# Kernel tuning notes

Measured on AMD Instinct MI355X. Metric: run time of the kernel, lower is better.

## Reference

```python
import jax, jax.numpy as jnp
import numpy as np

KH, KW = 2, 2          # kernel_size
STH, STW = 2, 2        # stride
NW = KH * KW           # num wires (qubits) per patch
DIM = 2 ** NW          # Hilbert-space dim = 16


def setup_inputs() -> dict:
    key = jax.random.key(0)
    k1, k2 = jax.random.split(key)
    x = jax.random.normal(k1, (32, 4, 64, 64), dtype=jnp.float32)
    # learned parameter: [in_channels, out_channels//numwires, 2^NW, 2^NW]
    params = jax.random.normal(k2, (4, 8, DIM, DIM), dtype=jnp.float32)
    return {"x": x, "params": params}


def _extract_patches(x):
    # x: [B, C, H, W] -> [B, C, px, py, KH*KW] (row-major kh,kw ordering,
    # matching patches.permute(0,1,4,5,2,3).flatten(4) in the original)
    B, C, H, W = x.shape
    px = (H - KH) // STH + 1
    py = (W - KW) // STW + 1
    rows = (jnp.arange(px) * STH)[:, None] + jnp.arange(KH)  # [px, KH]
    cols = (jnp.arange(py) * STW)[:, None] + jnp.arange(KW)  # [py, KW]
    p = x[:, :, rows][:, :, :, :, cols]        # [B, C, px, KH, py, KW]
    p = p.transpose(0, 1, 2, 4, 3, 5)          # [B, C, px, py, KH, KW]
    return p.reshape(B, C, px, py, NW), px, py


def _forward(x, params):
    B, C, H, W = x.shape
    p, px, py = _extract_patches(x)
    M = B * px * py
    theta = p.transpose(1, 0, 2, 3, 4).reshape(C, M, NW)  # 'b c px py i -> c (b px py) i'

    # Encode: the original builds the full tensor-product of per-wire RX
    # matrices and contracts with |0...0>, which selects row 0 of the Kronecker
    # product. Row 0 of RX(theta) is [cos(t/2), -i sin(t/2)], so the encoded
    # state is the Kronecker product of the per-wire row-0 vectors (same math,
    # without materializing the [C,M,16,16] unitary).
    half = theta * 0.5
    v = (jnp.cos(half).astype(jnp.complex64)[..., None] * jnp.array([1.0, 0.0], jnp.complex64)
         + jnp.sin(half).astype(jnp.complex64)[..., None] * jnp.array([0.0, -1.0j], jnp.complex64))  # [C,M,NW,2]
    state = v[:, :, 0]                                     # [C, M, 2]
    for w in range(1, NW):
        state = (state[..., :, None] * v[:, :, w][..., None, :]).reshape(C, M, -1)
    # state: [C, M, DIM]

    # Skew-Hermitian generator: real part antisymmetric, imag part symmetric.
    sym = params + params.swapaxes(-1, -2)
    asym = params - params.swapaxes(-1, -2)
    SH = asym.astype(jnp.complex64) + 1j * sym.astype(jnp.complex64)  # [C, D, DIM, DIM]
    U = jax.vmap(jax.vmap(jax.scipy.linalg.expm))(SH)                 # [C, D, DIM, DIM]

    y = jnp.einsum('cdij,cmi->cdmj', U, state)  # [C, D, M, DIM]

    # Decode: per-wire marginal probabilities -> <sigma_z>-style expectation -> acos
    probs = (y * jnp.conj(y)).real              # [C, D, M, DIM]
    D = probs.shape[1]
    outs = []
    for j in range(NW):
        marg = probs.reshape(C, D, M, 2 ** j, 2, 2 ** (NW - j - 1)).sum(axis=(3, 5))  # [C,D,M,2]
        outs.append(jnp.arccos(marg[..., 0] - marg[..., 1]))
    out = jnp.stack(outs, -1)                   # [C, D, M, NW]
    out = out.sum(0)                            # [D, M, NW]  (sum over in_channels)

    # 'c (b px py) (x y) -> b (c x y) px py' with c=D, x=KH, y=KW
    out = out.reshape(D, B, px, py, KH, KW).transpose(1, 0, 4, 5, 2, 3)
    return out.reshape(B, D * KH * KW, px, py)  # [B, out_channels, px, py]


def reference(x, params):
    return _forward(x, params)
```

## Files before the change

### kernel.cpp

```cpp
#include <hip/hip_runtime.h>
#include <math.h>


#define TAYLOR_N 9

typedef __attribute__((ext_vector_type(8)))  short bf16x8;
typedef __attribute__((ext_vector_type(16))) float f32x16;

__device__ __forceinline__ unsigned bfr(float x) {
    unsigned u = __float_as_uint(x);
    return (u + 0x7FFFu + ((u >> 16) & 1u)) >> 16;
}

__global__ __launch_bounds__(256) void prep_kernel(const float* __restrict__ params,
                                                   unsigned* __restrict__ wfrag) {
    __shared__ float2 X[256];
    __shared__ float2 P0[256];
    __shared__ float2 P1[256];
    __shared__ float red[256];
    __shared__ float srow[16];
    __shared__ int ssexp;

    const int bid = blockIdx.x;
    const int tid = threadIdx.x;
    const int i = tid >> 4, j = tid & 15;

    const float* pm = params + bid * 256;
    float pij = pm[i * 16 + j];
    float pji = pm[j * 16 + i];
    float ar = pij - pji;
    float ai = pij + pji;
    red[tid] = fabsf(ar) + fabsf(ai);
    __syncthreads();
    if (j == 0) {
        float s = 0.f;
        for (int t = 0; t < 16; ++t) s += red[i * 16 + t];
        srow[i] = s;
    }
    __syncthreads();
    if (tid == 0) {
        float mx = 0.f;
        for (int t = 0; t < 16; ++t) mx = fmaxf(mx, srow[t]);
        int se = 0;
        while (mx > 0.5f && se < 40) { mx *= 0.5f; se++; }
        ssexp = se;
    }
    __syncthreads();
    const int sexp = ssexp;
    const float scale = exp2f((float)(-sexp));
    const float xr = ar * scale, xi = ai * scale;
    X[tid] = make_float2(xr, xi);
    float2 p = make_float2(xr / TAYLOR_N + ((i == j) ? 1.f : 0.f), xi / TAYLOR_N);
    P0[tid] = p;
    __syncthreads();

    float2 Xr[16];
    #pragma unroll
    for (int t = 0; t < 16; ++t) Xr[t] = X[i * 16 + t];

    float2* cur = P0;
    float2* nxt = P1;
    for (int k = TAYLOR_N - 1; k >= 1; --k) {
        float accr = 0.f, acci = 0.f;
        #pragma unroll
        for (int t = 0; t < 16; ++t) {
            float2 a = Xr[t];
            float2 bb = cur[t * 16 + j];
            accr += a.x * bb.x - a.y * bb.y;
            acci += a.x * bb.y + a.y * bb.x;
        }
        float inv = 1.f / (float)k;
        float2 np = make_float2(accr * inv + ((i == j) ? 1.f : 0.f), acci * inv);
        __syncthreads();
        nxt[tid] = np;
        __syncthreads();
        float2* tmp = cur; cur = nxt; nxt = tmp;
    }
    for (int sq = 0; sq < sexp; ++sq) {
        float accr = 0.f, acci = 0.f;
        #pragma unroll
        for (int t = 0; t < 16; ++t) {
            float2 a = cur[i * 16 + t];
            float2 bb = cur[t * 16 + j];
            accr += a.x * bb.x - a.y * bb.y;
            acci += a.x * bb.y + a.y * bb.x;
        }
        __syncthreads();
        nxt[tid] = make_float2(accr, acci);
        __syncthreads();
        float2* tmp = cur; cur = nxt; nxt = tmp;
    }
    float2 e = cur[tid];
    int pc = __popc(i) & 3;
    float2 o;
    if (pc == 0)      o = make_float2( e.x,  e.y);
    else if (pc == 1) o = make_float2( e.y, -e.x);
    else if (pc == 2) o = make_float2(-e.x, -e.y);
    else              o = make_float2(-e.y,  e.x);
    __syncthreads();
    X[(tid & 15) * 16 + (tid >> 4)] = o;
    __syncthreads();

    {
        const int lane = tid & 63;
        const int pr = tid >> 6;
        const int row = lane & 31;
        const int kh = lane >> 5;
        const int k0 = kh * 8 + pr * 2;
        float v0, v1;
        if (row < 16) { v0 = X[row * 16 + k0].x; v1 = X[row * 16 + k0 + 1].x; }
        else          { v0 = X[(row - 16) * 16 + k0].y; v1 = X[(row - 16) * 16 + k0 + 1].y; }
        unsigned base = (unsigned)(bid * 64 + lane) * 4u;
        wfrag[base + pr] = bfr(v0) | (bfr(v1) << 16);
    }
}

__device__ __forceinline__ float acos_fast(float t) {
    float ax = fabsf(t);
    float p = fmaf(ax, -0.0187293f, 0.0742610f);
    p = fmaf(ax, p, -0.2121144f);
    p = fmaf(ax, p, 1.5707288f);
    float f = sqrtf(1.0f - ax) * p;
    return (t >= 0.f) ? f : (3.14159265358979f - f);
}

__global__ __launch_bounds__(256)
__attribute__((amdgpu_waves_per_eu(2, 4)))
void qconv_kernel(const float* __restrict__ x,
                  const unsigned* __restrict__ wfrag,
                  float* __restrict__ out) {
    const int tid = threadIdx.x;
    const int lane = tid & 63;
    const int s = lane & 31;
    const int hi = lane >> 5;
    const int wave = blockIdx.x * 4 + (tid >> 6);
    const int msite = wave >> 1;
    const int dh = wave & 1;
    const int m = msite * 32 + s;
    const int b = m >> 10, ix = (m >> 5) & 31, iy = m & 31;

    const bf16x8* wf = (const bf16x8*)wfrag;

    bf16x8 bhi[4], blo[4];
    #pragma unroll
    for (int c = 0; c < 4; ++c) {
        const float* xc = x + (((b * 4 + c) * 64 + 2 * ix) * 64 + 2 * iy);
        float2 xa = *(const float2*)xc;
        float2 xb = *(const float2*)(xc + 64);
        float sn0, cs0, sn1, cs1, sn2, cs2, sn3, cs3;
        __sincosf(xa.x * 0.5f, &sn0, &cs0);
        __sincosf(xa.y * 0.5f, &sn1, &cs1);
        __sincosf(xb.x * 0.5f, &sn2, &cs2);
        __sincosf(xb.y * 0.5f, &sn3, &cs3);
        float f0 = hi ? sn0 : cs0;
        float g0 = f0 * cs1, g1 = f0 * sn1;
        float h0 = g0 * cs2, h1 = g0 * sn2, h2 = g1 * cs2, h3 = g1 * sn2;
        float r[8];
        r[0] = h0 * cs3; r[1] = h0 * sn3; r[2] = h1 * cs3; r[3] = h1 * sn3;
        r[4] = h2 * cs3; r[5] = h2 * sn3; r[6] = h3 * cs3; r[7] = h3 * sn3;
        #pragma unroll
        for (int e = 0; e < 8; ++e) {
            unsigned hb = bfr(r[e]);
            bhi[c][e] = (short)hb;
            blo[c][e] = (short)bfr(r[e] - __uint_as_float(hb << 16));
        }
    }

    const float sgn1 = hi ? -1.f : 1.f;
    const f32x16 z = {0.f,0.f,0.f,0.f,0.f,0.f,0.f,0.f,
                      0.f,0.f,0.f,0.f,0.f,0.f,0.f,0.f};

    #pragma unroll 1
    for (int dd = 0; dd < 4; ++dd) {
        const int d = dh * 4 + dd;
        float accA = 0.f, accB = 0.f;
        #pragma unroll
        for (int c = 0; c < 4; ++c) {
            const int cd = c * 8 + d;
            bf16x8 ahi = wf[cd * 64 + lane];
            f32x16 acc = __builtin_amdgcn_mfma_f32_32x32x16_bf16(ahi, blo[c], z, 0, 0, 0);
            acc = __builtin_amdgcn_mfma_f32_32x32x16_bf16(ahi, bhi[c], acc, 0, 0, 0);
            float q[8];
            #pragma unroll
            for (int i = 0; i < 8; ++i)
                q[i] = fmaf(acc[i], acc[i], acc[8 + i] * acc[8 + i]);
            float e01 = q[0] + q[1], o01 = q[0] - q[1];
            float e23 = q[2] + q[3], o23 = q[2] - q[3];
            float e45 = q[4] + q[5], o45 = q[4] - q[5];
            float e67 = q[6] + q[7], o67 = q[6] - q[7];
            float A  = e01 + e23, B2a = e01 - e23, A3a = o01 + o23;
            float C  = e45 + e67, B2b = e45 - e67, A3b = o45 + o67;
            float S   = A + C;
            float pw0 = A - C;
            float pw1 = sgn1 * S;
            float pw2 = B2a + B2b;
            float pw3 = A3a + A3b;
            float sendA = hi ? pw0 : pw2, myA = hi ? pw2 : pw0;
            float sendB = hi ? pw1 : pw3, myB = hi ? pw3 : pw1;
            float tA = myA + __shfl_xor(sendA, 32);
            float tB = myB + __shfl_xor(sendB, 32);
            tA = fminf(fmaxf(tA, -1.f), 1.f);
            tB = fminf(fmaxf(tB, -1.f), 1.f);
            accA += acos_fast(tA);
            accB += acos_fast(tB);
        }
        float* ob = out + ((b * 32 + d * 4 + 2 * hi) * 32 + ix) * 32 + iy;
        ob[0]    = accA;
        ob[1024] = accB;
    }
}

extern "C" void kernel_launch(void* const* d_in, const int* in_sizes, int n_in,
                              void* d_out, int out_size, void* d_ws, size_t ws_size,
                              hipStream_t stream) {
    const float* x = (const float*)d_in[0];
    const float* params = (const float*)d_in[1];
    float* out = (float*)d_out;
    unsigned* wfrag = (unsigned*)d_ws;

    prep_kernel<<<32, 256, 0, stream>>>(params, wfrag);
    qconv_kernel<<<512, 256, 0, stream>>>(x, wfrag, out);
}
```

Before: 23.42 us.

## Use Paterson-Stockmeyer Taylor expm and preload weight fragments in registers

The prep kernel's matrix exponential moves from a 9-term Horner Taylor series with a scaling threshold of 0.5 to a degree-12 Paterson-Stockmeyer evaluation built from X^2, X^3, X^4 with a threshold of 1.0. This cuts the number of serial 16x16 complex matmuls and barriers, and redundant syncs in the squaring loop are dropped. The main kernel issues all x loads and all 16 weight-fragment loads up front and fully unrolls the d loop, so load latency overlaps with the sincos work. The cost is higher register pressure in the main kernel and a change in the exponential's approximation error.

```diff
diff --git a/kernel.cpp b/kernel.cpp
--- a/kernel.cpp
+++ b/kernel.cpp
@@ -1,8 +1,6 @@
 #include <hip/hip_runtime.h>
 #include <math.h>
 
-
-#define TAYLOR_N 9
 
 typedef __attribute__((ext_vector_type(8)))  short bf16x8;
 typedef __attribute__((ext_vector_type(16))) float f32x16;
@@ -12,11 +10,42 @@
     return (u + 0x7FFFu + ((u >> 16) & 1u)) >> 16;
 }
 
+__device__ __forceinline__ void mm16(float2* D, const float2* A, const float2* B,
+                                     int i, int j, int tid) {
+    float accr = 0.f, acci = 0.f;
+    #pragma unroll
+    for (int t = 0; t < 16; ++t) {
+        float2 a = A[i * 16 + t], b = B[t * 16 + j];
+        accr += a.x * b.x - a.y * b.y;
+        acci += a.x * b.y + a.y * b.x;
+    }
+    D[tid] = make_float2(accr, acci);
+    __syncthreads();
+}
+
+__device__ __forceinline__ void mm16_addb(float2* D, const float2* A, const float2* B,
+                                          const float2* X1, const float2* X2c,
+                                          const float2* X3c,
+                                          float b0, float b1, float b2, float b3,
+                                          int i, int j, int tid) {
+    float accr = 0.f, acci = 0.f;
+    #pragma unroll
+    for (int t = 0; t < 16; ++t) {
+        float2 a = A[i * 16 + t], b = B[t * 16 + j];
+        accr += a.x * b.x - a.y * b.y;
+        acci += a.x * b.y + a.y * b.x;
+    }
+    float2 v1 = X1[tid], v2 = X2c[tid], v3 = X3c[tid];
+    float idd = (i == j) ? 1.f : 0.f;
+    accr += b0 * idd + b1 * v1.x + b2 * v2.x + b3 * v3.x;
+    acci +=            b1 * v1.y + b2 * v2.y + b3 * v3.y;
+    D[tid] = make_float2(accr, acci);
+    __syncthreads();
+}
+
 __global__ __launch_bounds__(256) void prep_kernel(const float* __restrict__ params,
                                                    unsigned* __restrict__ wfrag) {
-    __shared__ float2 X[256];
-    __shared__ float2 P0[256];
-    __shared__ float2 P1[256];
+    __shared__ float2 Xs[256], X2[256], X3[256], X4[256], PA[256], PB[256];
     __shared__ float red[256];
     __shared__ float srow[16];
     __shared__ int ssexp;
@@ -42,54 +71,48 @@
         float mx = 0.f;
         for (int t = 0; t < 16; ++t) mx = fmaxf(mx, srow[t]);
         int se = 0;
-        while (mx > 0.5f && se < 40) { mx *= 0.5f; se++; }
+        while (mx > 1.0f && se < 40) { mx *= 0.5f; se++; }
         ssexp = se;
     }
     __syncthreads();
     const int sexp = ssexp;
     const float scale = exp2f((float)(-sexp));
-    const float xr = ar * scale, xi = ai * scale;
-    X[tid] = make_float2(xr, xi);
-    float2 p = make_float2(xr / TAYLOR_N + ((i == j) ? 1.f : 0.f), xi / TAYLOR_N);
-    P0[tid] = p;
-    __syncthreads();
-
-    float2 Xr[16];
-    #pragma unroll
-    for (int t = 0; t < 16; ++t) Xr[t] = X[i * 16 + t];
-
-    float2* cur = P0;
-    float2* nxt = P1;
-    for (int k = TAYLOR_N - 1; k >= 1; --k) {
-        float accr = 0.f, acci = 0.f;
-        #pragma unroll
-        for (int t = 0; t < 16; ++t) {
-            float2 a = Xr[t];
-            float2 bb = cur[t * 16 + j];
-            accr += a.x * bb.x - a.y * bb.y;
-            acci += a.x * bb.y + a.y * bb.x;
-        }
-        float inv = 1.f / (float)k;
-        float2 np = make_float2(accr * inv + ((i == j) ? 1.f : 0.f), acci * inv);
+    Xs[tid] = make_float2(ar * scale, ai * scale);
+    __syncthreads();
+
+    mm16(X2, Xs, Xs, i, j, tid);
+    mm16(X3, X2, Xs, i, j, tid);
+    mm16(X4, X2, X2, i, j, tid);
+
+    {
+        const float c8 = 2.4801587e-5f, c9 = 2.7557319e-6f, c10 = 2.7557319e-7f,
+                    c11 = 2.5052108e-8f, c12 = 2.0876757e-9f;
+        float2 v1 = Xs[tid], v2 = X2[tid], v3 = X3[tid], v4 = X4[tid];
+        float idd = (i == j) ? 1.f : 0.f;
+        PA[tid] = make_float2(c8 * idd + c9 * v1.x + c10 * v2.x + c11 * v3.x + c12 * v4.x,
+                              c9 * v1.y + c10 * v2.y + c11 * v3.y + c12 * v4.y);
         __syncthreads();
-        nxt[tid] = np;
-        __syncthreads();
-        float2* tmp = cur; cur = nxt; nxt = tmp;
-    }
+    }
+    mm16_addb(PB, X4, PA, Xs, X2, X3,
+              4.1666667e-2f, 8.3333333e-3f, 1.3888889e-3f, 1.9841270e-4f, i, j, tid);
+    mm16_addb(PA, X4, PB, Xs, X2, X3,
+              1.f, 1.f, 0.5f, 1.6666667e-1f, i, j, tid);
+
+    float2* cur = PA;
+    float2* nxt = PB;
     for (int sq = 0; sq < sexp; ++sq) {
         float accr = 0.f, acci = 0.f;
         #pragma unroll
         for (int t = 0; t < 16; ++t) {
-            float2 a = cur[i * 16 + t];
-            float2 bb = cur[t * 16 + j];
-            accr += a.x * bb.x - a.y * bb.y;
-            acci += a.x * bb.y + a.y * bb.x;
+            float2 a = cur[i * 16 + t], b = cur[t * 16 + j];
+            accr += a.x * b.x - a.y * b.y;
+            acci += a.x * b.y + a.y * b.x;
         }
-        __syncthreads();
         nxt[tid] = make_float2(accr, acci);
         __syncthreads();
         float2* tmp = cur; cur = nxt; nxt = tmp;
     }
+
     float2 e = cur[tid];
     int pc = __popc(i) & 3;
     float2 o;
@@ -97,8 +120,7 @@
     else if (pc == 1) o = make_float2( e.y, -e.x);
     else if (pc == 2) o = make_float2(-e.x, -e.y);
     else              o = make_float2(-e.y,  e.x);
-    __syncthreads();
-    X[(tid & 15) * 16 + (tid >> 4)] = o;
+    Xs[(tid & 15) * 16 + (tid >> 4)] = o;
     __syncthreads();
 
     {
@@ -108,8 +130,8 @@
         const int kh = lane >> 5;
         const int k0 = kh * 8 + pr * 2;
         float v0, v1;
-        if (row < 16) { v0 = X[row * 16 + k0].x; v1 = X[row * 16 + k0 + 1].x; }
-        else          { v0 = X[(row - 16) * 16 + k0].y; v1 = X[(row - 16) * 16 + k0 + 1].y; }
+        if (row < 16) { v0 = Xs[row * 16 + k0].x; v1 = Xs[row * 16 + k0 + 1].x; }
+        else          { v0 = Xs[(row - 16) * 16 + k0].y; v1 = Xs[(row - 16) * 16 + k0 + 1].y; }
         unsigned base = (unsigned)(bid * 64 + lane) * 4u;
         wfrag[base + pr] = bfr(v0) | (bfr(v1) << 16);
     }
@@ -141,17 +163,28 @@
 
     const bf16x8* wf = (const bf16x8*)wfrag;
 
-    bf16x8 bhi[4], blo[4];
+    float2 xa[4], xb[4];
     #pragma unroll
     for (int c = 0; c < 4; ++c) {
         const float* xc = x + (((b * 4 + c) * 64 + 2 * ix) * 64 + 2 * iy);
-        float2 xa = *(const float2*)xc;
-        float2 xb = *(const float2*)(xc + 64);
+        xa[c] = *(const float2*)xc;
+        xb[c] = *(const float2*)(xc + 64);
+    }
+    bf16x8 wfr[16];
+    #pragma unroll
+    for (int dd = 0; dd < 4; ++dd)
+        #pragma unroll
+        for (int c = 0; c < 4; ++c)
+            wfr[dd * 4 + c] = wf[(c * 8 + dh * 4 + dd) * 64 + lane];
+
+    bf16x8 bhi[4], blo[4];
+    #pragma unroll
+    for (int c = 0; c < 4; ++c) {
         float sn0, cs0, sn1, cs1, sn2, cs2, sn3, cs3;
-        __sincosf(xa.x * 0.5f, &sn0, &cs0);
-        __sincosf(xa.y * 0.5f, &sn1, &cs1);
-        __sincosf(xb.x * 0.5f, &sn2, &cs2);
-        __sincosf(xb.y * 0.5f, &sn3, &cs3);
+        __sincosf(xa[c].x * 0.5f, &sn0, &cs0);
+        __sincosf(xa[c].y * 0.5f, &sn1, &cs1);
+        __sincosf(xb[c].x * 0.5f, &sn2, &cs2);
+        __sincosf(xb[c].y * 0.5f, &sn3, &cs3);
         float f0 = hi ? sn0 : cs0;
         float g0 = f0 * cs1, g1 = f0 * sn1;
         float h0 = g0 * cs2, h1 = g0 * sn2, h2 = g1 * cs2, h3 = g1 * sn2;
@@ -170,14 +203,13 @@
     const f32x16 z = {0.f,0.f,0.f,0.f,0.f,0.f,0.f,0.f,
                       0.f,0.f,0.f,0.f,0.f,0.f,0.f,0.f};
 
-    #pragma unroll 1
+    #pragma unroll
     for (int dd = 0; dd < 4; ++dd) {
         const int d = dh * 4 + dd;
         float accA = 0.f, accB = 0.f;
         #pragma unroll
         for (int c = 0; c < 4; ++c) {
-            const int cd = c * 8 + d;
-            bf16x8 ahi = wf[cd * 64 + lane];
+            bf16x8 ahi = wfr[dd * 4 + c];
             f32x16 acc = __builtin_amdgcn_mfma_f32_32x32x16_bf16(ahi, blo[c], z, 0, 0, 0);
             acc = __builtin_amdgcn_mfma_f32_32x32x16_bf16(ahi, bhi[c], acc, 0, 0, 0);
             float q[8];
```

Result: faster. 21.52 us (-8.1%).
